# Performance work log

Measured on AMD Instinct MI355X. Metric: run time of the kernel, lower is better.

Reference implementation:

```python
import jax, jax.numpy as jnp
import numpy as np

B, M, N, DC = 32, 4096, 8192, 10
NUM_ITERS = 8
TEMP = 0.01      # smooth_min temperature
ALPHA = 100.0    # smooth_sign sharpness
BIG = 100000000.0


def setup_inputs() -> dict:
    rng = np.random.default_rng(0)
    # regular Tanner graph: each check connects to DC distinct variables
    chk_nbrs = np.argpartition(rng.random((M, N)), DC, axis=1)[:, :DC].astype(np.int32)
    p = rng.uniform(1e-3, 0.05, N)
    prior_llr = np.log((1.0 - p) / p).astype(np.float32)
    gamma = (0.1 * rng.standard_normal(N)).astype(np.float32)
    syndromes = rng.integers(0, 2, size=(B, M)).astype(np.float32)
    return {
        "syndromes": jnp.asarray(syndromes),
        "prior_llr": jnp.asarray(prior_llr),
        "gamma": jnp.asarray(gamma),
        "chk_nbrs": jnp.asarray(chk_nbrs),
    }


def _bp(syndromes, prior_llr, gamma, chk_nbrs):
    b = syndromes.shape[0]
    m, dc = chk_nbrs.shape
    n = prior_llr.shape[0]
    eye = jnp.eye(dc, dtype=bool)                      # (dc, dc)
    syn_sgn = 1.0 - 2.0 * syndromes                    # (b, m)
    var_flat = chk_nbrs.reshape(-1)                    # (m*dc,)

    def check_update(v2c):
        # v2c: (b, m, dc) messages var->check along each check's edge list
        s = jnp.tanh(ALPHA * v2c)                      # smooth_sign
        a = jnp.abs(v2c)
        # leave-one-out product of signs: mask diagonal with 1.0
        prod_excl = jnp.prod(jnp.where(eye, 1.0, s[:, :, None, :]), axis=-1)   # (b, m, dc)
        # leave-one-out smooth_min: mask diagonal with BIG, softmin-weighted sum
        a_m = jnp.where(eye, BIG, a[:, :, None, :])                            # (b, m, dc, dc)
        min_excl = jnp.sum(a_m * jax.nn.softmax(-a_m / TEMP, axis=-1), axis=-1)
        return syn_sgn[:, :, None] * prod_excl * min_excl                      # (b, m, dc)

    def scatter_to_vars(c2v):
        # sum of incoming check->var messages per variable: (b, n)
        return jnp.zeros((b, n), c2v.dtype).at[:, var_flat].add(c2v.reshape(b, -1))

    # initial v2c messages = prior LLR of the source variable
    v2c = jnp.broadcast_to(prior_llr[chk_nbrs], (b, m, dc))

    # iteration 0: no memory term
    c2v = check_update(v2c)
    llrs = scatter_to_vars(c2v) + prior_llr[None, :]
    v2c = llrs[:, chk_nbrs] - c2v

    def step(carry, _):
        v2c, llrs = carry
        c2v = check_update(v2c)
        llrs = scatter_to_vars(c2v) + (1.0 - gamma)[None, :] * prior_llr[None, :] + gamma[None, :] * llrs
        v2c = llrs[:, chk_nbrs] - c2v
        return (v2c, llrs), None

    (_, llrs), _ = jax.lax.scan(jax.checkpoint(step), (v2c, llrs), None, length=NUM_ITERS - 1)
    return llrs


def reference(syndromes, prior_llr, gamma, chk_nbrs):
    return _bp(syndromes, prior_llr, gamma, chk_nbrs)
```

## Files before the change

kernel.cpp:

```cpp
#include <hip/hip_runtime.h>

#define B 32
#define M 4096
#define N 8192
#define DC 10
#define NUM_ITERS 8
#define INV_TEMP 100.0f
#define ALPHA 100.0f
#define NB (N * B)
#define MB (M * B)

__global__ __launch_bounds__(256) void prologue_kernel(
    const float* __restrict__ syn,
    const float* __restrict__ prior,
    const float* __restrict__ gamma,
    float* __restrict__ accumA,
    float* __restrict__ L0,
    float* __restrict__ L1,
    float* __restrict__ syn_t,
    float* __restrict__ pg)
{
    int idx = blockIdx.x * blockDim.x + threadIdx.x;
    if (idx < NB) {
        float p = prior[idx >> 5];
        accumA[idx] = 0.0f;
        L0[idx] = p;
        L1[idx] = p;
    }
    if (idx < MB) {
        int b = idx & 31, m = idx >> 5;
        syn_t[idx] = 1.0f - 2.0f * syn[(size_t)b * M + m];
    }
    if (idx < N) pg[idx] = (1.0f - gamma[idx]) * prior[idx];
}

template <int KIND>
__global__ __launch_bounds__(256) void check_kernel(
    const float* __restrict__ syn_t,
    const float* __restrict__ prior,
    const float* __restrict__ pg,
    const float* __restrict__ gamma,
    const int*   __restrict__ nbrs,
    const float* __restrict__ R,
    float*       __restrict__ W,
    float*       __restrict__ Z,
    const float* __restrict__ Lold,
    float*       __restrict__ Lnew,
    float*       __restrict__ c2v)
{
    int idx = blockIdx.x * blockDim.x + threadIdx.x;
    if (idx >= MB) return;
    const int b = idx & 31;
    const int m = idx >> 5;

    Z[idx] = 0.0f;
    Z[idx + MB] = 0.0f;

    const int* nr = nbrs + m * DC;
    float* c2vp = c2v + (size_t)(m * DC) * B + b;

    int nb[DC];
    #pragma unroll
    for (int i = 0; i < DC; ++i) nb[i] = nr[i];

    float v[DC];
    if (KIND == 0) {
        #pragma unroll
        for (int i = 0; i < DC; ++i) v[i] = prior[nb[i]];
    } else if (KIND == 1) {
        #pragma unroll
        for (int i = 0; i < DC; ++i) {
            int g = nb[i] * B + b;
            float l = R[g] + prior[nb[i]];
            Lnew[g] = l;
            v[i] = l - c2vp[(size_t)i * B];
        }
    } else {
        #pragma unroll
        for (int i = 0; i < DC; ++i) {
            int g = nb[i] * B + b;
            float l = R[g] + pg[nb[i]] + gamma[nb[i]] * Lold[g];
            Lnew[g] = l;
            v[i] = l - c2vp[(size_t)i * B];
        }
    }

    float s[DC], a[DC];
    #pragma unroll
    for (int i = 0; i < DC; ++i) {
        a[i] = fabsf(v[i]);
        float t = __expf(-2.0f * ALPHA * a[i]);
        float mag = (1.0f - t) / (1.0f + t);
        s[i] = copysignf(mag, v[i]);
    }

    float min1 = 3.4e38f, min2 = 3.4e38f;
    int am = 0;
    #pragma unroll
    for (int i = 0; i < DC; ++i) {
        if (a[i] < min1) { min2 = min1; min1 = a[i]; am = i; }
        else if (a[i] < min2) { min2 = a[i]; }
    }

    float pre[DC + 1], suf[DC + 1];
    pre[0] = 1.0f;
    #pragma unroll
    for (int i = 0; i < DC; ++i) pre[i + 1] = pre[i] * s[i];
    suf[DC] = 1.0f;
    #pragma unroll
    for (int i = DC - 1; i >= 0; --i) suf[i] = suf[i + 1] * s[i];

    float w[DC];
    float se = 0.0f, sae = 0.0f;
    #pragma unroll
    for (int i = 0; i < DC; ++i) {
        w[i] = __expf((min1 - a[i]) * INV_TEMP);
        se  += w[i];
        sae += a[i] * w[i];
    }

    float se2 = 0.0f, sae2 = 0.0f;
    #pragma unroll
    for (int j = 0; j < DC; ++j) {
        float e2 = __expf((min2 - a[j]) * INV_TEMP);
        e2 = (j != am) ? e2 : 0.0f;
        se2  += e2;
        sae2 += a[j] * e2;
    }
    float me_am = sae2 / se2;

    float ssgn = syn_t[idx];

    #pragma unroll
    for (int i = 0; i < DC; ++i) {
        float me = (i == am) ? me_am : (sae - a[i] * w[i]) / (se - w[i]);
        float out = ssgn * (pre[i] * suf[i + 1]) * me;
        c2vp[(size_t)i * B] = out;
        atomicAdd(&W[nb[i] * B + b], out);
    }
}

__global__ __launch_bounds__(256) void final_kernel(
    const float* __restrict__ R,
    const float* __restrict__ pg,
    const float* __restrict__ gamma,
    const float* __restrict__ Lold,
    float*       __restrict__ out)
{
    int idx = blockIdx.x * blockDim.x + threadIdx.x;
    if (idx >= NB) return;
    int n = idx & (N - 1);
    int b = idx >> 13;
    int goff = n * B + b;
    out[idx] = R[goff] + pg[n] + gamma[n] * Lold[goff];
}

extern "C" void kernel_launch(void* const* d_in, const int* in_sizes, int n_in,
                              void* d_out, int out_size, void* d_ws, size_t ws_size,
                              hipStream_t stream) {
    const float* syn   = (const float*)d_in[0];
    const float* prior = (const float*)d_in[1];
    const float* gamma = (const float*)d_in[2];
    const int*   nbrs  = (const int*)d_in[3];
    float* out = (float*)d_out;

    float* ws = (float*)d_ws;
    float* A[3] = { ws, ws + NB, ws + 2 * (size_t)NB };
    float* L[2] = { ws + 3 * (size_t)NB, ws + 4 * (size_t)NB };
    float* c2v   = ws + 5 * (size_t)NB;
    float* syn_t = c2v + (size_t)M * DC * B;
    float* pg    = syn_t + MB;

    dim3 blk256(256);
    dim3 pgrid((NB + 255) / 256);
    dim3 cgrid((MB + 255) / 256);

    prologue_kernel<<<pgrid, blk256, 0, stream>>>(syn, prior, gamma, A[0], L[0], L[1], syn_t, pg);

    for (int t = 0; t < NUM_ITERS; ++t) {
        float* Rb = A[(t + 2) % 3];
        float* Wb = A[t % 3];
        float* Zb = A[(t + 1) % 3];
        float* Lo = L[t & 1];
        float* Ln = L[(t + 1) & 1];
        if (t == 0) {
            check_kernel<0><<<cgrid, blk256, 0, stream>>>(syn_t, prior, pg, gamma, nbrs,
                                                          nullptr, Wb, Zb, nullptr, nullptr, c2v);
        } else if (t == 1) {
            check_kernel<1><<<cgrid, blk256, 0, stream>>>(syn_t, prior, pg, gamma, nbrs,
                                                          Rb, Wb, Zb, nullptr, Ln, c2v);
        } else {
            check_kernel<2><<<cgrid, blk256, 0, stream>>>(syn_t, prior, pg, gamma, nbrs,
                                                          Rb, Wb, Zb, Lo, Ln, c2v);
        }
    }
    final_kernel<<<pgrid, blk256, 0, stream>>>(A[1], pg, gamma, L[0], out);
}
```

Baseline: 85.83 us.

## Interleave accumulator and LLR into float2 and write LLR once per variable

Packs each variable's check-message accumulator and previous LLR into one float2, so the gather reads both with a single 8-byte load instead of two separate arrays. A one-time claim kernel picks a single owning edge per variable, and only that edge writes the recomputed LLR. Before, every incident check wrote it redundantly. The cost is two extra small setup kernels' worth of work and wider strided atomics and stores on float2 elements.

```diff
diff --git a/kernel.cpp b/kernel.cpp
--- a/kernel.cpp
+++ b/kernel.cpp
@@ -9,54 +9,66 @@
 #define ALPHA 100.0f
 #define NB (N * B)
 #define MB (M * B)
+#define NEDGE (M * DC)
+
 
 __global__ __launch_bounds__(256) void prologue_kernel(
     const float* __restrict__ syn,
     const float* __restrict__ prior,
     const float* __restrict__ gamma,
-    float* __restrict__ accumA,
-    float* __restrict__ L0,
-    float* __restrict__ L1,
-    float* __restrict__ syn_t,
-    float* __restrict__ pg)
+    float2* __restrict__ P0, float2* __restrict__ P1, float2* __restrict__ P2,
+    float*  __restrict__ syn_t,
+    float*  __restrict__ pg,
+    int*    __restrict__ claim,
+    int*    __restrict__ ownbits)
 {
     int idx = blockIdx.x * blockDim.x + threadIdx.x;
     if (idx < NB) {
-        float p = prior[idx >> 5];
-        accumA[idx] = 0.0f;
-        L0[idx] = p;
-        L1[idx] = p;
+        float2 init = make_float2(0.0f, prior[idx >> 5]);
+        P0[idx] = init; P1[idx] = init; P2[idx] = init;
     }
     if (idx < MB) {
         int b = idx & 31, m = idx >> 5;
         syn_t[idx] = 1.0f - 2.0f * syn[(size_t)b * M + m];
     }
-    if (idx < N) pg[idx] = (1.0f - gamma[idx]) * prior[idx];
+    if (idx < N) { pg[idx] = (1.0f - gamma[idx]) * prior[idx]; claim[idx] = 0; }
+    if (idx < M) ownbits[idx] = 0;
+}
+
+__global__ __launch_bounds__(256) void claim_kernel(
+    const int* __restrict__ nbrs,
+    int* __restrict__ claim,
+    int* __restrict__ ownbits)
+{
+    int e = blockIdx.x * blockDim.x + threadIdx.x;
+    if (e >= NEDGE) return;
+    if (atomicExch(&claim[nbrs[e]], 1) == 0)
+        atomicOr(&ownbits[e / DC], 1 << (e % DC));
 }
 
 template <int KIND>
 __global__ __launch_bounds__(256) void check_kernel(
-    const float* __restrict__ syn_t,
-    const float* __restrict__ prior,
-    const float* __restrict__ pg,
-    const float* __restrict__ gamma,
-    const int*   __restrict__ nbrs,
-    const float* __restrict__ R,
-    float*       __restrict__ W,
-    float*       __restrict__ Z,
-    const float* __restrict__ Lold,
-    float*       __restrict__ Lnew,
-    float*       __restrict__ c2v)
+    const float*  __restrict__ syn_t,
+    const float*  __restrict__ prior,
+    const float*  __restrict__ pg,
+    const float*  __restrict__ gamma,
+    const int*    __restrict__ nbrs,
+    const int*    __restrict__ ownbits,
+    const float2* __restrict__ Pr,
+    float2*       __restrict__ Pw,
+    float2*       __restrict__ Pz,
+    float*        __restrict__ c2v)
 {
     int idx = blockIdx.x * blockDim.x + threadIdx.x;
     if (idx >= MB) return;
     const int b = idx & 31;
     const int m = idx >> 5;
 
-    Z[idx] = 0.0f;
-    Z[idx + MB] = 0.0f;
+    Pz[idx].x = 0.0f;
+    Pz[idx + MB].x = 0.0f;
 
     const int* nr = nbrs + m * DC;
+    const int ow = ownbits[m];
     float* c2vp = c2v + (size_t)(m * DC) * B + b;
 
     int nb[DC];
@@ -67,20 +79,15 @@
     if (KIND == 0) {
         #pragma unroll
         for (int i = 0; i < DC; ++i) v[i] = prior[nb[i]];
-    } else if (KIND == 1) {
-        #pragma unroll
-        for (int i = 0; i < DC; ++i) {
-            int g = nb[i] * B + b;
-            float l = R[g] + prior[nb[i]];
-            Lnew[g] = l;
-            v[i] = l - c2vp[(size_t)i * B];
-        }
     } else {
         #pragma unroll
         for (int i = 0; i < DC; ++i) {
-            int g = nb[i] * B + b;
-            float l = R[g] + pg[nb[i]] + gamma[nb[i]] * Lold[g];
-            Lnew[g] = l;
+            const int g = nb[i] * B + b;
+            float2 rl = Pr[g];
+            float l;
+            if (KIND == 1) l = rl.x + prior[nb[i]];
+            else           l = rl.x + pg[nb[i]] + gamma[nb[i]] * rl.y;
+            if ((ow >> i) & 1) Pw[g].y = l;
             v[i] = l - c2vp[(size_t)i * B];
         }
     }
@@ -89,8 +96,8 @@
     #pragma unroll
     for (int i = 0; i < DC; ++i) {
         a[i] = fabsf(v[i]);
-        float t = __expf(-2.0f * ALPHA * a[i]);
-        float mag = (1.0f - t) / (1.0f + t);
+        float tt = __expf(-2.0f * ALPHA * a[i]);
+        float mag = (1.0f - tt) / (1.0f + tt);
         s[i] = copysignf(mag, v[i]);
     }
 
@@ -136,23 +143,22 @@
         float me = (i == am) ? me_am : (sae - a[i] * w[i]) / (se - w[i]);
         float out = ssgn * (pre[i] * suf[i + 1]) * me;
         c2vp[(size_t)i * B] = out;
-        atomicAdd(&W[nb[i] * B + b], out);
+        atomicAdd(&Pw[nb[i] * B + b].x, out);
     }
 }
 
 __global__ __launch_bounds__(256) void final_kernel(
-    const float* __restrict__ R,
-    const float* __restrict__ pg,
-    const float* __restrict__ gamma,
-    const float* __restrict__ Lold,
-    float*       __restrict__ out)
+    const float2* __restrict__ Pr,
+    const float*  __restrict__ pg,
+    const float*  __restrict__ gamma,
+    float*        __restrict__ out)
 {
     int idx = blockIdx.x * blockDim.x + threadIdx.x;
     if (idx >= NB) return;
     int n = idx & (N - 1);
     int b = idx >> 13;
-    int goff = n * B + b;
-    out[idx] = R[goff] + pg[n] + gamma[n] * Lold[goff];
+    float2 rl = Pr[n * B + b];
+    out[idx] = rl.x + pg[n] + gamma[n] * rl.y;
 }
 
 extern "C" void kernel_launch(void* const* d_in, const int* in_sizes, int n_in,
@@ -164,35 +170,41 @@
     const int*   nbrs  = (const int*)d_in[3];
     float* out = (float*)d_out;
 
-    float* ws = (float*)d_ws;
-    float* A[3] = { ws, ws + NB, ws + 2 * (size_t)NB };
-    float* L[2] = { ws + 3 * (size_t)NB, ws + 4 * (size_t)NB };
-    float* c2v   = ws + 5 * (size_t)NB;
-    float* syn_t = c2v + (size_t)M * DC * B;
-    float* pg    = syn_t + MB;
-
-    dim3 blk256(256);
+    char* ws = (char*)d_ws;
+    float2* P[3];
+    P[0] = (float2*)ws;
+    P[1] = P[0] + NB;
+    P[2] = P[1] + NB;
+    float* c2v    = (float*)(P[2] + NB);
+    float* syn_t  = c2v + (size_t)NEDGE * B;
+    float* pg     = syn_t + MB;
+    int*   claim  = (int*)(pg + N);
+    int*   ownbits= claim + N;
+
+    dim3 blk(256);
     dim3 pgrid((NB + 255) / 256);
+    dim3 egrid((NEDGE + 255) / 256);
     dim3 cgrid((MB + 255) / 256);
 
-    prologue_kernel<<<pgrid, blk256, 0, stream>>>(syn, prior, gamma, A[0], L[0], L[1], syn_t, pg);
+    prologue_kernel<<<pgrid, blk, 0, stream>>>(syn, prior, gamma,
+                                               P[0], P[1], P[2], syn_t, pg,
+                                               claim, ownbits);
+    claim_kernel<<<egrid, blk, 0, stream>>>(nbrs, claim, ownbits);
 
     for (int t = 0; t < NUM_ITERS; ++t) {
-        float* Rb = A[(t + 2) % 3];
-        float* Wb = A[t % 3];
-        float* Zb = A[(t + 1) % 3];
-        float* Lo = L[t & 1];
-        float* Ln = L[(t + 1) & 1];
+        float2* Pr = P[(t + 2) % 3];
+        float2* Pw = P[t % 3];
+        float2* Pz = P[(t + 1) % 3];
         if (t == 0) {
-            check_kernel<0><<<cgrid, blk256, 0, stream>>>(syn_t, prior, pg, gamma, nbrs,
-                                                          nullptr, Wb, Zb, nullptr, nullptr, c2v);
+            check_kernel<0><<<cgrid, blk, 0, stream>>>(syn_t, prior, pg, gamma, nbrs,
+                                                       ownbits, Pr, Pw, Pz, c2v);
         } else if (t == 1) {
-            check_kernel<1><<<cgrid, blk256, 0, stream>>>(syn_t, prior, pg, gamma, nbrs,
-                                                          Rb, Wb, Zb, nullptr, Ln, c2v);
+            check_kernel<1><<<cgrid, blk, 0, stream>>>(syn_t, prior, pg, gamma, nbrs,
+                                                       ownbits, Pr, Pw, Pz, c2v);
         } else {
-            check_kernel<2><<<cgrid, blk256, 0, stream>>>(syn_t, prior, pg, gamma, nbrs,
-                                                          Rb, Wb, Zb, Lo, Ln, c2v);
+            check_kernel<2><<<cgrid, blk, 0, stream>>>(syn_t, prior, pg, gamma, nbrs,
+                                                       ownbits, Pr, Pw, Pz, c2v);
         }
     }
-    final_kernel<<<pgrid, blk256, 0, stream>>>(A[1], pg, gamma, L[0], out);
-}
+    final_kernel<<<pgrid, blk, 0, stream>>>(P[1], pg, gamma, out);
+}
```

Measured after the change: 136.9 us. 59.5% more time.

## Store per-edge LLR alongside c2v to drop per-iteration scattered L writes

Applied to the files above, without the earlier changes.

Replaces the double-buffered per-variable LLR arrays with a per-edge float2 buffer holding (c2v, llr) for each edge, so each check thread reads the previous LLR from its own contiguous edge slot instead of gathering Lold. The scattered Lnew write is removed except in the final iteration, where the single L buffer is written for the final kernel. This trades the random per-variable reads and writes for wider coalesced edge loads and stores. It relies on every edge of a variable computing the same LLR value.

```diff
diff --git a/kernel.cpp b/kernel.cpp
--- a/kernel.cpp
+++ b/kernel.cpp
@@ -9,23 +9,21 @@
 #define ALPHA 100.0f
 #define NB (N * B)
 #define MB (M * B)
+#define NEDGE (M * DC)
 
 __global__ __launch_bounds__(256) void prologue_kernel(
     const float* __restrict__ syn,
     const float* __restrict__ prior,
     const float* __restrict__ gamma,
     float* __restrict__ accumA,
-    float* __restrict__ L0,
-    float* __restrict__ L1,
+    float* __restrict__ L,
     float* __restrict__ syn_t,
     float* __restrict__ pg)
 {
     int idx = blockIdx.x * blockDim.x + threadIdx.x;
     if (idx < NB) {
-        float p = prior[idx >> 5];
         accumA[idx] = 0.0f;
-        L0[idx] = p;
-        L1[idx] = p;
+        L[idx] = prior[idx >> 5];
     }
     if (idx < MB) {
         int b = idx & 31, m = idx >> 5;
@@ -34,19 +32,18 @@
     if (idx < N) pg[idx] = (1.0f - gamma[idx]) * prior[idx];
 }
 
-template <int KIND>
+template <int KIND, bool WL>
 __global__ __launch_bounds__(256) void check_kernel(
-    const float* __restrict__ syn_t,
-    const float* __restrict__ prior,
-    const float* __restrict__ pg,
-    const float* __restrict__ gamma,
-    const int*   __restrict__ nbrs,
-    const float* __restrict__ R,
-    float*       __restrict__ W,
-    float*       __restrict__ Z,
-    const float* __restrict__ Lold,
-    float*       __restrict__ Lnew,
-    float*       __restrict__ c2v)
+    const float*  __restrict__ syn_t,
+    const float*  __restrict__ prior,
+    const float*  __restrict__ pg,
+    const float*  __restrict__ gamma,
+    const int*    __restrict__ nbrs,
+    const float*  __restrict__ R,
+    float*        __restrict__ W,
+    float*        __restrict__ Z,
+    float*        __restrict__ L,
+    float2*       __restrict__ S)
 {
     int idx = blockIdx.x * blockDim.x + threadIdx.x;
     if (idx >= MB) return;
@@ -57,31 +54,27 @@
     Z[idx + MB] = 0.0f;
 
     const int* nr = nbrs + m * DC;
-    float* c2vp = c2v + (size_t)(m * DC) * B + b;
+    float2* Sp = S + (size_t)(m * DC) * B + b;
 
     int nb[DC];
     #pragma unroll
     for (int i = 0; i < DC; ++i) nb[i] = nr[i];
 
-    float v[DC];
+    float v[DC], lv[DC];
     if (KIND == 0) {
         #pragma unroll
-        for (int i = 0; i < DC; ++i) v[i] = prior[nb[i]];
-    } else if (KIND == 1) {
-        #pragma unroll
-        for (int i = 0; i < DC; ++i) {
-            int g = nb[i] * B + b;
-            float l = R[g] + prior[nb[i]];
-            Lnew[g] = l;
-            v[i] = l - c2vp[(size_t)i * B];
-        }
+        for (int i = 0; i < DC; ++i) { v[i] = prior[nb[i]]; lv[i] = v[i]; }
     } else {
         #pragma unroll
         for (int i = 0; i < DC; ++i) {
-            int g = nb[i] * B + b;
-            float l = R[g] + pg[nb[i]] + gamma[nb[i]] * Lold[g];
-            Lnew[g] = l;
-            v[i] = l - c2vp[(size_t)i * B];
+            float2 st = Sp[(size_t)i * B];
+            const int g = nb[i] * B + b;
+            float l;
+            if (KIND == 1) l = R[g] + prior[nb[i]];
+            else           l = R[g] + pg[nb[i]] + gamma[nb[i]] * st.y;
+            if (WL) L[g] = l;
+            lv[i] = l;
+            v[i] = l - st.x;
         }
     }
 
@@ -89,8 +82,8 @@
     #pragma unroll
     for (int i = 0; i < DC; ++i) {
         a[i] = fabsf(v[i]);
-        float t = __expf(-2.0f * ALPHA * a[i]);
-        float mag = (1.0f - t) / (1.0f + t);
+        float tt = __expf(-2.0f * ALPHA * a[i]);
+        float mag = (1.0f - tt) / (1.0f + tt);
         s[i] = copysignf(mag, v[i]);
     }
 
@@ -135,7 +128,7 @@
     for (int i = 0; i < DC; ++i) {
         float me = (i == am) ? me_am : (sae - a[i] * w[i]) / (se - w[i]);
         float out = ssgn * (pre[i] * suf[i + 1]) * me;
-        c2vp[(size_t)i * B] = out;
+        Sp[(size_t)i * B] = make_float2(out, lv[i]);
         atomicAdd(&W[nb[i] * B + b], out);
     }
 }
@@ -144,7 +137,7 @@
     const float* __restrict__ R,
     const float* __restrict__ pg,
     const float* __restrict__ gamma,
-    const float* __restrict__ Lold,
+    const float* __restrict__ L,
     float*       __restrict__ out)
 {
     int idx = blockIdx.x * blockDim.x + threadIdx.x;
@@ -152,7 +145,7 @@
     int n = idx & (N - 1);
     int b = idx >> 13;
     int goff = n * B + b;
-    out[idx] = R[goff] + pg[n] + gamma[n] * Lold[goff];
+    out[idx] = R[goff] + pg[n] + gamma[n] * L[goff];
 }
 
 extern "C" void kernel_launch(void* const* d_in, const int* in_sizes, int n_in,
@@ -166,33 +159,34 @@
 
     float* ws = (float*)d_ws;
     float* A[3] = { ws, ws + NB, ws + 2 * (size_t)NB };
-    float* L[2] = { ws + 3 * (size_t)NB, ws + 4 * (size_t)NB };
-    float* c2v   = ws + 5 * (size_t)NB;
-    float* syn_t = c2v + (size_t)M * DC * B;
-    float* pg    = syn_t + MB;
+    float* L    = ws + 3 * (size_t)NB;
+    float* syn_t= L + NB;
+    float* pg   = syn_t + MB;
+    float2* S   = (float2*)(pg + N);
 
-    dim3 blk256(256);
+    dim3 blk(256);
     dim3 pgrid((NB + 255) / 256);
     dim3 cgrid((MB + 255) / 256);
 
-    prologue_kernel<<<pgrid, blk256, 0, stream>>>(syn, prior, gamma, A[0], L[0], L[1], syn_t, pg);
+    prologue_kernel<<<pgrid, blk, 0, stream>>>(syn, prior, gamma, A[0], L, syn_t, pg);
 
     for (int t = 0; t < NUM_ITERS; ++t) {
         float* Rb = A[(t + 2) % 3];
         float* Wb = A[t % 3];
         float* Zb = A[(t + 1) % 3];
-        float* Lo = L[t & 1];
-        float* Ln = L[(t + 1) & 1];
         if (t == 0) {
-            check_kernel<0><<<cgrid, blk256, 0, stream>>>(syn_t, prior, pg, gamma, nbrs,
-                                                          nullptr, Wb, Zb, nullptr, nullptr, c2v);
+            check_kernel<0, false><<<cgrid, blk, 0, stream>>>(syn_t, prior, pg, gamma, nbrs,
+                                                              Rb, Wb, Zb, L, S);
         } else if (t == 1) {
-            check_kernel<1><<<cgrid, blk256, 0, stream>>>(syn_t, prior, pg, gamma, nbrs,
-                                                          Rb, Wb, Zb, nullptr, Ln, c2v);
+            check_kernel<1, false><<<cgrid, blk, 0, stream>>>(syn_t, prior, pg, gamma, nbrs,
+                                                              Rb, Wb, Zb, L, S);
+        } else if (t < NUM_ITERS - 1) {
+            check_kernel<2, false><<<cgrid, blk, 0, stream>>>(syn_t, prior, pg, gamma, nbrs,
+                                                              Rb, Wb, Zb, L, S);
         } else {
-            check_kernel<2><<<cgrid, blk256, 0, stream>>>(syn_t, prior, pg, gamma, nbrs,
-                                                          Rb, Wb, Zb, Lo, Ln, c2v);
+            check_kernel<2, true><<<cgrid, blk, 0, stream>>>(syn_t, prior, pg, gamma, nbrs,
+                                                             Rb, Wb, Zb, L, S);
         }
     }
-    final_kernel<<<pgrid, blk256, 0, stream>>>(A[1], pg, gamma, L[0], out);
+    final_kernel<<<pgrid, blk, 0, stream>>>(A[1], pg, gamma, L, out);
 }
```

New measurement: 84.08 us. -2.0%, faster.
